# Kernel optimization log

Measured on AMD Instinct MI355X. Metric: run time of the kernel, lower is better.

Reference implementation:

```python
import jax, jax.numpy as jnp
import numpy as np

NUM_CLASSES = 1000  # label range; segment count for the per-class reduction


def setup_inputs() -> dict:
    key = jax.random.key(0)
    k1, k2, k3 = jax.random.split(key, 3)
    B, C = 32768, NUM_CLASSES
    f1 = jax.random.normal(k1, (B, C), dtype=jnp.float32)
    f2 = jax.random.normal(k2, (B, C), dtype=jnp.float32)
    label = jax.random.randint(k3, (B,), 0, NUM_CLASSES, dtype=jnp.int64)
    return {"f1": f1, "f2": f2, "label": label}


def reference(f1, f2, label):
    # log p = log_softmax(f1), t = softmax(f2); pointwise KL term t*(log t - log p)
    C = f1.shape[1]
    logp = jax.nn.log_softmax(f1, axis=1)
    logt = jax.nn.log_softmax(f2, axis=1)
    t = jnp.exp(logt)
    row_kl = jnp.sum(t * (logt - logp), axis=1)  # [B] per-row KL sum
    # Per-class grouping: torch version concatenates n_l rows into a flat
    # [n_l*C] vector and applies KLDivLoss(batchmean) -> divide by n_l*C.
    seg_kl = jax.ops.segment_sum(row_kl, label, num_segments=NUM_CLASSES)
    cnt = jax.ops.segment_sum(jnp.ones_like(row_kl), label, num_segments=NUM_CLASSES)
    per_class = jnp.where(cnt > 0, seg_kl / (cnt * C), 0.0)
    return jnp.sum(per_class)
```

## Files before the change

kernel.cpp:

```cpp
#include <hip/hip_runtime.h>
#include <cfloat>
#include <math.h>

#define NCLS 1000
#define VEC (NCLS / 4)

__global__ __launch_bounds__(256) void rowkl_kernel(
    const float* __restrict__ f1, const float* __restrict__ f2,
    const int* __restrict__ label,
    float* __restrict__ seg, float* __restrict__ cnt) {
  __shared__ float lds[20];
  const int row = blockIdx.x;
  const int t = threadIdx.x;
  const float4* r1 = reinterpret_cast<const float4*>(f1 + (size_t)row * NCLS);
  const float4* r2 = reinterpret_cast<const float4*>(f2 + (size_t)row * NCLS);
  const bool valid = (t < VEC);

  float4 a = make_float4(0.f, 0.f, 0.f, 0.f);
  float4 b = make_float4(0.f, 0.f, 0.f, 0.f);
  if (valid) { a = r1[t]; b = r2[t]; }

  float m1 = valid ? fmaxf(fmaxf(a.x, a.y), fmaxf(a.z, a.w)) : -FLT_MAX;
  float m2 = valid ? fmaxf(fmaxf(b.x, b.y), fmaxf(b.z, b.w)) : -FLT_MAX;

  #pragma unroll
  for (int o = 32; o >= 1; o >>= 1) {
    m1 = fmaxf(m1, __shfl_xor(m1, o));
    m2 = fmaxf(m2, __shfl_xor(m2, o));
  }
  const int wid = t >> 6;
  if ((t & 63) == 0) { lds[wid] = m1; lds[4 + wid] = m2; }
  __syncthreads();
  m1 = fmaxf(fmaxf(lds[0], lds[1]), fmaxf(lds[2], lds[3]));
  m2 = fmaxf(fmaxf(lds[4], lds[5]), fmaxf(lds[6], lds[7]));

  float e1 = 0.f, e2 = 0.f, T = 0.f;
  if (valid) {
    e1 = __expf(a.x - m1) + __expf(a.y - m1) + __expf(a.z - m1) + __expf(a.w - m1);
    const float t0 = __expf(b.x - m2), t1 = __expf(b.y - m2);
    const float t2 = __expf(b.z - m2), t3 = __expf(b.w - m2);
    e2 = t0 + t1 + t2 + t3;
    T = t0 * (b.x - a.x) + t1 * (b.y - a.y) + t2 * (b.z - a.z) + t3 * (b.w - a.w);
  }
  #pragma unroll
  for (int o = 32; o >= 1; o >>= 1) {
    e1 += __shfl_xor(e1, o);
    e2 += __shfl_xor(e2, o);
    T  += __shfl_xor(T, o);
  }
  if ((t & 63) == 0) { lds[8 + wid] = e1; lds[12 + wid] = e2; lds[16 + wid] = T; }
  __syncthreads();
  if (t == 0) {
    e1 = lds[8]  + lds[9]  + lds[10] + lds[11];
    e2 = lds[12] + lds[13] + lds[14] + lds[15];
    T  = lds[16] + lds[17] + lds[18] + lds[19];
    const float rkl = T / e2 - ((m2 - m1) + __logf(e2) - __logf(e1));
    const int l = label[row];
    atomicAdd(&seg[l], rkl);
    atomicAdd(&cnt[l], 1.0f);
  }
}

__global__ __launch_bounds__(256) void finalize_kernel(
    const float* __restrict__ seg, const float* __restrict__ cnt,
    float* __restrict__ out) {
  __shared__ float lds[4];
  float s = 0.f;
  for (int c = threadIdx.x; c < NCLS; c += 256) {
    const float n = cnt[c];
    if (n > 0.f) s += seg[c] / (n * (float)NCLS);
  }
  #pragma unroll
  for (int o = 32; o >= 1; o >>= 1) s += __shfl_xor(s, o);
  const int wid = threadIdx.x >> 6;
  if ((threadIdx.x & 63) == 0) lds[wid] = s;
  __syncthreads();
  if (threadIdx.x == 0) out[0] = lds[0] + lds[1] + lds[2] + lds[3];
}

extern "C" void kernel_launch(void* const* d_in, const int* in_sizes, int n_in,
                              void* d_out, int out_size, void* d_ws, size_t ws_size,
                              hipStream_t stream) {
  const float* f1 = (const float*)d_in[0];
  const float* f2 = (const float*)d_in[1];
  const int* label = (const int*)d_in[2];
  float* seg = (float*)d_ws;
  float* cnt = seg + NCLS;

  hipMemsetAsync(d_ws, 0, 2 * NCLS * sizeof(float), stream);

  const int B = in_sizes[0] / NCLS;
  rowkl_kernel<<<B, 256, 0, stream>>>(f1, f2, label, seg, cnt);
  finalize_kernel<<<1, 256, 0, stream>>>(seg, cnt, (float*)d_out);
}
```

Before: 275.2 us.

## Map one row per wave, write per-row KL, and segment-reduce in LDS

The row kernel now assigns one row per 64-lane wave, with each lane holding four float4 chunks. This drops the LDS round-trips and __syncthreads barriers, and no lane sits idle for lack of data. Instead of issuing two global float atomics per row, it writes the per-row KL to a workspace array. A single 1024-thread finalize block then accumulates segment sums and counts with shared-memory atomics, which also removes the memset. The cost is a serial single-block pass over all 32768 rows at the end and a small extra global write and read.

```diff
diff --git a/kernel.cpp b/kernel.cpp
--- a/kernel.cpp
+++ b/kernel.cpp
@@ -7,75 +7,92 @@
 
 __global__ __launch_bounds__(256) void rowkl_kernel(
     const float* __restrict__ f1, const float* __restrict__ f2,
-    const int* __restrict__ label,
-    float* __restrict__ seg, float* __restrict__ cnt) {
-  __shared__ float lds[20];
-  const int row = blockIdx.x;
-  const int t = threadIdx.x;
+    float* __restrict__ rowkl, int B) {
+  const int wave = threadIdx.x >> 6;
+  const int lane = threadIdx.x & 63;
+  const int row = blockIdx.x * 4 + wave;
+  if (row >= B) return;
+
   const float4* r1 = reinterpret_cast<const float4*>(f1 + (size_t)row * NCLS);
   const float4* r2 = reinterpret_cast<const float4*>(f2 + (size_t)row * NCLS);
-  const bool valid = (t < VEC);
 
-  float4 a = make_float4(0.f, 0.f, 0.f, 0.f);
-  float4 b = make_float4(0.f, 0.f, 0.f, 0.f);
-  if (valid) { a = r1[t]; b = r2[t]; }
+  float4 a[4], b[4];
+  #pragma unroll
+  for (int j = 0; j < 4; ++j) {
+    const int idx = lane + 64 * j;
+    if (idx < VEC) {
+      a[j] = r1[idx];
+      b[j] = r2[idx];
+    } else {
+      a[j] = make_float4(-1e30f, -1e30f, -1e30f, -1e30f);
+      b[j] = make_float4(-1e30f, -1e30f, -1e30f, -1e30f);
+    }
+  }
 
-  float m1 = valid ? fmaxf(fmaxf(a.x, a.y), fmaxf(a.z, a.w)) : -FLT_MAX;
-  float m2 = valid ? fmaxf(fmaxf(b.x, b.y), fmaxf(b.z, b.w)) : -FLT_MAX;
-
+  float m1 = -FLT_MAX, m2 = -FLT_MAX;
   #pragma unroll
-  for (int o = 32; o >= 1; o >>= 1) {
-    m1 = fmaxf(m1, __shfl_xor(m1, o));
-    m2 = fmaxf(m2, __shfl_xor(m2, o));
-  }
-  const int wid = t >> 6;
-  if ((t & 63) == 0) { lds[wid] = m1; lds[4 + wid] = m2; }
-  __syncthreads();
-  m1 = fmaxf(fmaxf(lds[0], lds[1]), fmaxf(lds[2], lds[3]));
-  m2 = fmaxf(fmaxf(lds[4], lds[5]), fmaxf(lds[6], lds[7]));
-
-  float e1 = 0.f, e2 = 0.f, T = 0.f;
-  if (valid) {
-    e1 = __expf(a.x - m1) + __expf(a.y - m1) + __expf(a.z - m1) + __expf(a.w - m1);
-    const float t0 = __expf(b.x - m2), t1 = __expf(b.y - m2);
-    const float t2 = __expf(b.z - m2), t3 = __expf(b.w - m2);
-    e2 = t0 + t1 + t2 + t3;
-    T = t0 * (b.x - a.x) + t1 * (b.y - a.y) + t2 * (b.z - a.z) + t3 * (b.w - a.w);
+  for (int j = 0; j < 4; ++j) {
+    m1 = fmaxf(m1, fmaxf(fmaxf(a[j].x, a[j].y), fmaxf(a[j].z, a[j].w)));
+    m2 = fmaxf(m2, fmaxf(fmaxf(b[j].x, b[j].y), fmaxf(b[j].z, b[j].w)));
   }
   #pragma unroll
   for (int o = 32; o >= 1; o >>= 1) {
-    e1 += __shfl_xor(e1, o);
-    e2 += __shfl_xor(e2, o);
-    T  += __shfl_xor(T, o);
+    m1 = fmaxf(m1, __shfl_xor(m1, o, 64));
+    m2 = fmaxf(m2, __shfl_xor(m2, o, 64));
   }
-  if ((t & 63) == 0) { lds[8 + wid] = e1; lds[12 + wid] = e2; lds[16 + wid] = T; }
-  __syncthreads();
-  if (t == 0) {
-    e1 = lds[8]  + lds[9]  + lds[10] + lds[11];
-    e2 = lds[12] + lds[13] + lds[14] + lds[15];
-    T  = lds[16] + lds[17] + lds[18] + lds[19];
-    const float rkl = T / e2 - ((m2 - m1) + __logf(e2) - __logf(e1));
-    const int l = label[row];
-    atomicAdd(&seg[l], rkl);
-    atomicAdd(&cnt[l], 1.0f);
+
+  float e1 = 0.f, e2 = 0.f, T = 0.f;
+  #pragma unroll
+  for (int j = 0; j < 4; ++j) {
+    e1 += __expf(a[j].x - m1) + __expf(a[j].y - m1) +
+          __expf(a[j].z - m1) + __expf(a[j].w - m1);
+    const float t0 = __expf(b[j].x - m2), t1 = __expf(b[j].y - m2);
+    const float t2 = __expf(b[j].z - m2), t3 = __expf(b[j].w - m2);
+    e2 += t0 + t1 + t2 + t3;
+    T += t0 * (b[j].x - a[j].x) + t1 * (b[j].y - a[j].y) +
+         t2 * (b[j].z - a[j].z) + t3 * (b[j].w - a[j].w);
+  }
+  #pragma unroll
+  for (int o = 32; o >= 1; o >>= 1) {
+    e1 += __shfl_xor(e1, o, 64);
+    e2 += __shfl_xor(e2, o, 64);
+    T  += __shfl_xor(T, o, 64);
+  }
+
+  if (lane == 0) {
+    rowkl[row] = T / e2 - ((m2 - m1) + __logf(e2) - __logf(e1));
   }
 }
 
-__global__ __launch_bounds__(256) void finalize_kernel(
-    const float* __restrict__ seg, const float* __restrict__ cnt,
-    float* __restrict__ out) {
-  __shared__ float lds[4];
+__global__ __launch_bounds__(1024) void finalize_kernel(
+    const float* __restrict__ rowkl, const int* __restrict__ label,
+    float* __restrict__ out, int B) {
+  __shared__ float seg[NCLS];
+  __shared__ float cnt[NCLS];
+  __shared__ float wsum[16];
+  for (int c = threadIdx.x; c < NCLS; c += 1024) { seg[c] = 0.f; cnt[c] = 0.f; }
+  __syncthreads();
+  for (int r = threadIdx.x; r < B; r += 1024) {
+    const int l = label[r];
+    atomicAdd(&seg[l], rowkl[r]);
+    atomicAdd(&cnt[l], 1.0f);
+  }
+  __syncthreads();
   float s = 0.f;
-  for (int c = threadIdx.x; c < NCLS; c += 256) {
+  for (int c = threadIdx.x; c < NCLS; c += 1024) {
     const float n = cnt[c];
     if (n > 0.f) s += seg[c] / (n * (float)NCLS);
   }
   #pragma unroll
-  for (int o = 32; o >= 1; o >>= 1) s += __shfl_xor(s, o);
-  const int wid = threadIdx.x >> 6;
-  if ((threadIdx.x & 63) == 0) lds[wid] = s;
+  for (int o = 32; o >= 1; o >>= 1) s += __shfl_xor(s, o, 64);
+  if ((threadIdx.x & 63) == 0) wsum[threadIdx.x >> 6] = s;
   __syncthreads();
-  if (threadIdx.x == 0) out[0] = lds[0] + lds[1] + lds[2] + lds[3];
+  if (threadIdx.x == 0) {
+    float tot = 0.f;
+    #pragma unroll
+    for (int w = 0; w < 16; ++w) tot += wsum[w];
+    out[0] = tot;
+  }
 }
 
 extern "C" void kernel_launch(void* const* d_in, const int* in_sizes, int n_in,
@@ -84,12 +101,9 @@
   const float* f1 = (const float*)d_in[0];
   const float* f2 = (const float*)d_in[1];
   const int* label = (const int*)d_in[2];
-  float* seg = (float*)d_ws;
-  float* cnt = seg + NCLS;
-
-  hipMemsetAsync(d_ws, 0, 2 * NCLS * sizeof(float), stream);
+  float* rowkl = (float*)d_ws;
 
   const int B = in_sizes[0] / NCLS;
-  rowkl_kernel<<<B, 256, 0, stream>>>(f1, f2, label, seg, cnt);
-  finalize_kernel<<<1, 256, 0, stream>>>(seg, cnt, (float*)d_out);
+  rowkl_kernel<<<(B + 3) / 4, 256, 0, stream>>>(f1, f2, rowkl, B);
+  finalize_kernel<<<1, 1024, 0, stream>>>(rowkl, label, (float*)d_out, B);
 }
```

Measured after the change: 350.6 us. 27.4% more time.
